# Optimization experiments

Hardware: AMD Instinct MI355X
Metric: run time of the kernel (lower is better)

## Reference

```python
import jax, jax.numpy as jnp
import numpy as np

FP8_E4M3_MAX = 448.0  # max representable magnitude of float8_e4m3fn

def fake_quant_fp8(t):
    """Per-tensor dynamic-scale fp8 (e4m3) quantize + dequantize."""
    amax = jnp.max(jnp.abs(t))
    scale = FP8_E4M3_MAX / jnp.maximum(amax, 1e-12)
    q = (t * scale).astype(jnp.float8_e4m3fn).astype(jnp.float32)
    return q / scale

def setup_inputs() -> dict:
    key = jax.random.key(0)
    k1, k2, k3 = jax.random.split(key, 3)
    d_in, d_out = 1024, 1024
    x = jax.random.normal(k1, (4, 8192, d_in), dtype=jnp.float32)
    weight = jax.random.normal(k2, (d_out, d_in), dtype=jnp.float32) * (1.0 / np.sqrt(d_in))
    bias = jax.random.normal(k3, (d_out,), dtype=jnp.float32) * 0.01
    return {"x": x, "weight": weight, "bias": bias}

def reference(x, weight, bias):
    # fp8-quantized linear: quantize activations and weights to e4m3 with
    # per-tensor dynamic scales, matmul, dequant (folded into fake-quant), add bias.
    xq = fake_quant_fp8(x)        # [b, s, d_in]
    wq = fake_quant_fp8(weight)   # [d_out, d_in]
    return jnp.einsum('bsd,od->bso', xq, wq) + bias
```

## Files before the change

kernel.cpp:

```cpp
#include <hip/hip_runtime.h>
#include <stdint.h>

typedef float floatx4 __attribute__((ext_vector_type(4)));
typedef int intx8 __attribute__((ext_vector_type(8)));

#define FP8_MAX 448.0f
#define BM 128
#define BN 128
#define BK 128
#define GX 2048
#define GW 256

__global__ void amax_partial(const float* __restrict__ x, long n4x,
                             const float* __restrict__ w, long n4w,
                             float* __restrict__ part) {
    const float4* p4; long n4, i0, stride;
    if (blockIdx.x < GX) {
        p4 = (const float4*)x; n4 = n4x;
        i0 = (long)blockIdx.x * blockDim.x + threadIdx.x;
        stride = (long)GX * blockDim.x;
    } else {
        p4 = (const float4*)w; n4 = n4w;
        i0 = (long)(blockIdx.x - GX) * blockDim.x + threadIdx.x;
        stride = (long)GW * blockDim.x;
    }
    float m = 0.f;
    for (long i = i0; i < n4; i += stride) {
        float4 v = p4[i];
        m = fmaxf(m, fmaxf(fmaxf(fabsf(v.x), fabsf(v.y)),
                           fmaxf(fabsf(v.z), fabsf(v.w))));
    }
    #pragma unroll
    for (int off = 32; off > 0; off >>= 1) m = fmaxf(m, __shfl_down(m, off, 64));
    __shared__ float red[4];
    if ((threadIdx.x & 63) == 0) red[threadIdx.x >> 6] = m;
    __syncthreads();
    if (threadIdx.x == 0)
        part[blockIdx.x] = fmaxf(fmaxf(red[0], red[1]), fmaxf(red[2], red[3]));
}

__global__ void quantw_scales(const float* __restrict__ part,
                              const float* __restrict__ w, int4* __restrict__ wq,
                              long n16w, float* __restrict__ scales) {
    const int tid = threadIdx.x;
    float mx = 0.f, mw = 0.f;
    for (int i = tid; i < GX; i += 256) mx = fmaxf(mx, part[i]);
    for (int i = GX + tid; i < GX + GW; i += 256) mw = fmaxf(mw, part[i]);
    #pragma unroll
    for (int off = 32; off > 0; off >>= 1) {
        mx = fmaxf(mx, __shfl_down(mx, off, 64));
        mw = fmaxf(mw, __shfl_down(mw, off, 64));
    }
    __shared__ float rx[4], rw[4];
    if ((tid & 63) == 0) { rx[tid >> 6] = mx; rw[tid >> 6] = mw; }
    __syncthreads();
    const float ax = fmaxf(fmaxf(rx[0], rx[1]), fmaxf(rx[2], rx[3]));
    const float aw = fmaxf(fmaxf(rw[0], rw[1]), fmaxf(rw[2], rw[3]));
    const float sx = FP8_MAX / fmaxf(ax, 1e-12f);
    const float sw = FP8_MAX / fmaxf(aw, 1e-12f);
    if (blockIdx.x == 0 && tid == 0) {
        scales[0] = sx; scales[1] = sw; scales[2] = 1.0f / (sx * sw);
    }
    const float4* p4 = (const float4*)w;
    const long i = (long)blockIdx.x * 256 + tid;
    if (i < n16w) {
        float4 v0 = p4[i * 4 + 0];
        float4 v1 = p4[i * 4 + 1];
        float4 v2 = p4[i * 4 + 2];
        float4 v3 = p4[i * 4 + 3];
        int w0 = 0, w1 = 0, w2 = 0, w3 = 0;
        w0 = __builtin_amdgcn_cvt_pk_fp8_f32(v0.x * sw, v0.y * sw, w0, false);
        w0 = __builtin_amdgcn_cvt_pk_fp8_f32(v0.z * sw, v0.w * sw, w0, true);
        w1 = __builtin_amdgcn_cvt_pk_fp8_f32(v1.x * sw, v1.y * sw, w1, false);
        w1 = __builtin_amdgcn_cvt_pk_fp8_f32(v1.z * sw, v1.w * sw, w1, true);
        w2 = __builtin_amdgcn_cvt_pk_fp8_f32(v2.x * sw, v2.y * sw, w2, false);
        w2 = __builtin_amdgcn_cvt_pk_fp8_f32(v2.z * sw, v2.w * sw, w2, true);
        w3 = __builtin_amdgcn_cvt_pk_fp8_f32(v3.x * sw, v3.y * sw, w3, false);
        w3 = __builtin_amdgcn_cvt_pk_fp8_f32(v3.z * sw, v3.w * sw, w3, true);
        wq[i] = make_int4(w0, w1, w2, w3);
    }
}

__global__ __launch_bounds__(256) void gemm_fp8mx(
    const float* __restrict__ xf, const unsigned char* __restrict__ Bq,
    const float* __restrict__ bias, const float* __restrict__ scales,
    float* __restrict__ out, int M, int N, int K) {
    __shared__ __align__(16) unsigned char tA[BM * BK];
    __shared__ __align__(16) unsigned char tB[BN * BK];

    const int tid = threadIdx.x;
    const int lane = tid & 63;
    const int wave = tid >> 6;
    const int waveM = (wave & 1) * 64;
    const int waveN = (wave >> 1) * 64;

    const int nbx = gridDim.x;
    const int nwg = nbx * gridDim.y;
    int bx = blockIdx.x, by = blockIdx.y;
    if (nbx == 8 && (nwg & 7) == 0) {
        const int f   = by * 8 + bx;
        const int per = nwg >> 3;
        const int sw  = (f & 7) * per + (f >> 3);
        bx = sw & 7;
        by = sw >> 3;
    }
    const long m0 = (long)by * BM;
    const int n0 = bx * BN;

    const int srow = lane >> 3;
    const int sphys = lane & 7;

    const float sx = scales[0];
    const float inv = scales[2];

    floatx4 acc[4][4];
    #pragma unroll
    for (int i = 0; i < 4; ++i)
        #pragma unroll
        for (int j = 0; j < 4; ++j)
            acc[i][j] = (floatx4){0.f, 0.f, 0.f, 0.f};

    const int row16 = lane & 15;
    const int q2 = (lane >> 4) * 2;

    const float4* x4 = (const float4*)xf;
    const int K4 = K >> 2;

    for (int k0 = 0; k0 < K; k0 += BK) {
        __syncthreads();
        #pragma unroll
        for (int c = 0; c < 4; ++c) {
            const int r = wave * 32 + c * 8 + srow;
            const int lc = (sphys ^ (r & 7)) * 16;
            __builtin_amdgcn_global_load_lds(
                (const __attribute__((address_space(1))) void*)(Bq + (long)(n0 + r) * K + k0 + lc),
                (__attribute__((address_space(3))) void*)&tB[r * BK + sphys * 16], 16, 0, 0);
        }
        #pragma unroll
        for (int j = 0; j < 4; ++j) {
            const int fidx = (tid << 2) + (j << 10);
            const int row = fidx >> 5;
            const int c4 = fidx & 31;
            const float4* px = x4 + (m0 + row) * (long)K4 + (k0 >> 2) + c4;
            const float4 v0 = px[0];
            const float4 v1 = px[1];
            const float4 v2 = px[2];
            const float4 v3 = px[3];
            int w0 = 0, w1 = 0, w2 = 0, w3 = 0;
            w0 = __builtin_amdgcn_cvt_pk_fp8_f32(v0.x * sx, v0.y * sx, w0, false);
            w0 = __builtin_amdgcn_cvt_pk_fp8_f32(v0.z * sx, v0.w * sx, w0, true);
            w1 = __builtin_amdgcn_cvt_pk_fp8_f32(v1.x * sx, v1.y * sx, w1, false);
            w1 = __builtin_amdgcn_cvt_pk_fp8_f32(v1.z * sx, v1.w * sx, w1, true);
            w2 = __builtin_amdgcn_cvt_pk_fp8_f32(v2.x * sx, v2.y * sx, w2, false);
            w2 = __builtin_amdgcn_cvt_pk_fp8_f32(v2.z * sx, v2.w * sx, w2, true);
            w3 = __builtin_amdgcn_cvt_pk_fp8_f32(v3.x * sx, v3.y * sx, w3, false);
            w3 = __builtin_amdgcn_cvt_pk_fp8_f32(v3.z * sx, v3.w * sx, w3, true);
            const int phys = (tid & 7) ^ (row & 7);
            *(int4*)&tA[row * BK + phys * 16] = make_int4(w0, w1, w2, w3);
        }
        __syncthreads();

        intx8 af[4], bf[4];
        #pragma unroll
        for (int t = 0; t < 4; ++t) {
            const int row = waveM + t * 16 + row16;
            const int s = row & 7;
            const int4 lo = *(const int4*)&tA[row * BK + ((q2 ^ s)) * 16];
            const int4 hi = *(const int4*)&tA[row * BK + (((q2 + 1) ^ s)) * 16];
            af[t] = (intx8){lo.x, lo.y, lo.z, lo.w, hi.x, hi.y, hi.z, hi.w};
        }
        #pragma unroll
        for (int t = 0; t < 4; ++t) {
            const int row = waveN + t * 16 + row16;
            const int s = row & 7;
            const int4 lo = *(const int4*)&tB[row * BK + ((q2 ^ s)) * 16];
            const int4 hi = *(const int4*)&tB[row * BK + (((q2 + 1) ^ s)) * 16];
            bf[t] = (intx8){lo.x, lo.y, lo.z, lo.w, hi.x, hi.y, hi.z, hi.w};
        }
        #pragma unroll
        for (int mt = 0; mt < 4; ++mt)
            #pragma unroll
            for (int nt = 0; nt < 4; ++nt)
                acc[mt][nt] = __builtin_amdgcn_mfma_scale_f32_16x16x128_f8f6f4(
                    af[mt], bf[nt], acc[mt][nt], 0, 0,
                    0, 127, 0, 127);
    }

    const int col = lane & 15;
    const int rbase4 = (lane >> 4) * 4;
    #pragma unroll
    for (int nt = 0; nt < 4; ++nt) {
        const int gn = n0 + waveN + nt * 16 + col;
        const float bv = bias[gn];
        #pragma unroll
        for (int mt = 0; mt < 4; ++mt) {
            const long gm = m0 + waveM + mt * 16 + rbase4;
            float* po = out + gm * (long)N + gn;
            #pragma unroll
            for (int r = 0; r < 4; ++r)
                po[(long)r * N] = acc[mt][nt][r] * inv + bv;
        }
    }
}

extern "C" void kernel_launch(void* const* d_in, const int* in_sizes, int n_in,
                              void* d_out, int out_size, void* d_ws, size_t ws_size,
                              hipStream_t stream) {
    const float* x = (const float*)d_in[0];
    const float* w = (const float*)d_in[1];
    const float* bias = (const float*)d_in[2];
    float* out = (float*)d_out;

    const long nx = in_sizes[0];
    const long nw = in_sizes[1];
    const int N = in_sizes[2];
    const long K = nw / N;
    const long M = nx / K;

    unsigned char* ws = (unsigned char*)d_ws;
    unsigned char* wq = ws;
    float* part = (float*)(ws + nw);
    float* scales = (float*)(ws + nw + 16384);

    amax_partial<<<GX + GW, 256, 0, stream>>>(x, nx / 4, w, nw / 4, part);
    quantw_scales<<<GW, 256, 0, stream>>>(part, w, (int4*)wq, nw / 16, scales);

    dim3 grid(N / BN, (int)(M / BM));
    gemm_fp8mx<<<grid, 256, 0, stream>>>(x, wq, bias, scales, out,
                                         (int)M, N, (int)K);
}
```

Baseline: 314.9 us.

## Software-pipeline fp32 activation loads into registers one K-tile ahead

Prefetches the next K-tile of fp32 activations into 16 float4 registers while the current tile is converted to fp8, stored to LDS and consumed by MFMAs. The syncthreads calls are replaced by explicit s_barrier with a partial vmcnt wait, so the outstanding global prefetch loads stay in flight across the barrier. This hides global load latency behind compute at the cost of 64 extra VGPRs per thread, which may lower occupancy. The hand-written waitcnt must match the exact number of outstanding loads, which adds fragility.

Result: no change. 309.8 us (-1.6%).

```diff
diff --git a/kernel.cpp b/kernel.cpp
--- a/kernel.cpp
+++ b/kernel.cpp
@@ -126,8 +126,22 @@
     const float4* x4 = (const float4*)xf;
     const int K4 = K >> 2;
 
+    const int arow0 = tid >> 3;
+    const int ac4   = (tid & 7) * 4;
+    const int aphys = tid & 7;
+
+    float4 pre[16];
+    #pragma unroll
+    for (int j = 0; j < 4; ++j) {
+        const int row = arow0 + 32 * j;
+        const float4* px = x4 + (m0 + row) * (long)K4 + ac4;
+        pre[j * 4 + 0] = px[0];
+        pre[j * 4 + 1] = px[1];
+        pre[j * 4 + 2] = px[2];
+        pre[j * 4 + 3] = px[3];
+    }
+
     for (int k0 = 0; k0 < K; k0 += BK) {
-        __syncthreads();
         #pragma unroll
         for (int c = 0; c < 4; ++c) {
             const int r = wave * 32 + c * 8 + srow;
@@ -136,16 +150,14 @@
                 (const __attribute__((address_space(1))) void*)(Bq + (long)(n0 + r) * K + k0 + lc),
                 (__attribute__((address_space(3))) void*)&tB[r * BK + sphys * 16], 16, 0, 0);
         }
+        __builtin_amdgcn_sched_barrier(0);
+
         #pragma unroll
         for (int j = 0; j < 4; ++j) {
-            const int fidx = (tid << 2) + (j << 10);
-            const int row = fidx >> 5;
-            const int c4 = fidx & 31;
-            const float4* px = x4 + (m0 + row) * (long)K4 + (k0 >> 2) + c4;
-            const float4 v0 = px[0];
-            const float4 v1 = px[1];
-            const float4 v2 = px[2];
-            const float4 v3 = px[3];
+            const float4 v0 = pre[j * 4 + 0];
+            const float4 v1 = pre[j * 4 + 1];
+            const float4 v2 = pre[j * 4 + 2];
+            const float4 v3 = pre[j * 4 + 3];
             int w0 = 0, w1 = 0, w2 = 0, w3 = 0;
             w0 = __builtin_amdgcn_cvt_pk_fp8_f32(v0.x * sx, v0.y * sx, w0, false);
             w0 = __builtin_amdgcn_cvt_pk_fp8_f32(v0.z * sx, v0.w * sx, w0, true);
@@ -155,10 +167,26 @@
             w2 = __builtin_amdgcn_cvt_pk_fp8_f32(v2.z * sx, v2.w * sx, w2, true);
             w3 = __builtin_amdgcn_cvt_pk_fp8_f32(v3.x * sx, v3.y * sx, w3, false);
             w3 = __builtin_amdgcn_cvt_pk_fp8_f32(v3.z * sx, v3.w * sx, w3, true);
-            const int phys = (tid & 7) ^ (row & 7);
+            const int row = arow0 + 32 * j;
+            const int phys = aphys ^ (row & 7);
             *(int4*)&tA[row * BK + phys * 16] = make_int4(w0, w1, w2, w3);
         }
-        __syncthreads();
+        __builtin_amdgcn_sched_barrier(0);
+
+        const int kn4 = ((k0 + BK < K) ? (k0 + BK) : k0) >> 2;
+        #pragma unroll
+        for (int j = 0; j < 4; ++j) {
+            const int row = arow0 + 32 * j;
+            const float4* px = x4 + (m0 + row) * (long)K4 + kn4 + ac4;
+            pre[j * 4 + 0] = px[0];
+            pre[j * 4 + 1] = px[1];
+            pre[j * 4 + 2] = px[2];
+            pre[j * 4 + 3] = px[3];
+        }
+
+        asm volatile("s_waitcnt vmcnt(16) lgkmcnt(0)" ::: "memory");
+        __builtin_amdgcn_s_barrier();
+        __builtin_amdgcn_sched_barrier(0);
 
         intx8 af[4], bf[4];
         #pragma unroll
@@ -184,6 +212,9 @@
                 acc[mt][nt] = __builtin_amdgcn_mfma_scale_f32_16x16x128_f8f6f4(
                     af[mt], bf[nt], acc[mt][nt], 0, 0,
                     0, 127, 0, 127);
+
+        __builtin_amdgcn_s_barrier();
+        __builtin_amdgcn_sched_barrier(0);
     }
 
     const int col = lane & 15;
```

## Software-pipeline the fp8 GEMM main loop with double-buffered B and register-prefetched A

Applied to the files above, without the earlier changes.

Restructures the K loop into a two-stage software pipeline. The B tile is double-buffered in LDS via async global_load_lds, and the fp32 activation tiles are prefetched two iterations ahead into two register arrays (preA and preB). Explicit vmcnt waits, s_barrier and sched_barrier calls order the stages so that global loads overlap with conversion and MFMA work. This adds about 128 VGPRs of prefetch storage and an extra 16KB of LDS, which may lower occupancy, and it relies on a hand-counted vmcnt value. It also assumes the number of K tiles is even.

Result: slower. 351.4 us (+11.6%).

```diff
diff --git a/kernel.cpp b/kernel.cpp
--- a/kernel.cpp
+++ b/kernel.cpp
@@ -86,7 +86,8 @@
     const float* __restrict__ bias, const float* __restrict__ scales,
     float* __restrict__ out, int M, int N, int K) {
     __shared__ __align__(16) unsigned char tA[BM * BK];
-    __shared__ __align__(16) unsigned char tB[BN * BK];
+    __shared__ __align__(16) unsigned char tB0[BN * BK];
+    __shared__ __align__(16) unsigned char tB1[BN * BK];
 
     const int tid = threadIdx.x;
     const int lane = tid & 63;
@@ -125,66 +126,117 @@
 
     const float4* x4 = (const float4*)xf;
     const int K4 = K >> 2;
-
-    for (int k0 = 0; k0 < K; k0 += BK) {
-        __syncthreads();
-        #pragma unroll
-        for (int c = 0; c < 4; ++c) {
-            const int r = wave * 32 + c * 8 + srow;
-            const int lc = (sphys ^ (r & 7)) * 16;
-            __builtin_amdgcn_global_load_lds(
-                (const __attribute__((address_space(1))) void*)(Bq + (long)(n0 + r) * K + k0 + lc),
-                (__attribute__((address_space(3))) void*)&tB[r * BK + sphys * 16], 16, 0, 0);
-        }
-        #pragma unroll
-        for (int j = 0; j < 4; ++j) {
-            const int fidx = (tid << 2) + (j << 10);
-            const int row = fidx >> 5;
-            const int c4 = fidx & 31;
-            const float4* px = x4 + (m0 + row) * (long)K4 + (k0 >> 2) + c4;
-            const float4 v0 = px[0];
-            const float4 v1 = px[1];
-            const float4 v2 = px[2];
-            const float4 v3 = px[3];
-            int w0 = 0, w1 = 0, w2 = 0, w3 = 0;
-            w0 = __builtin_amdgcn_cvt_pk_fp8_f32(v0.x * sx, v0.y * sx, w0, false);
-            w0 = __builtin_amdgcn_cvt_pk_fp8_f32(v0.z * sx, v0.w * sx, w0, true);
-            w1 = __builtin_amdgcn_cvt_pk_fp8_f32(v1.x * sx, v1.y * sx, w1, false);
-            w1 = __builtin_amdgcn_cvt_pk_fp8_f32(v1.z * sx, v1.w * sx, w1, true);
-            w2 = __builtin_amdgcn_cvt_pk_fp8_f32(v2.x * sx, v2.y * sx, w2, false);
-            w2 = __builtin_amdgcn_cvt_pk_fp8_f32(v2.z * sx, v2.w * sx, w2, true);
-            w3 = __builtin_amdgcn_cvt_pk_fp8_f32(v3.x * sx, v3.y * sx, w3, false);
-            w3 = __builtin_amdgcn_cvt_pk_fp8_f32(v3.z * sx, v3.w * sx, w3, true);
-            const int phys = (tid & 7) ^ (row & 7);
-            *(int4*)&tA[row * BK + phys * 16] = make_int4(w0, w1, w2, w3);
-        }
-        __syncthreads();
-
-        intx8 af[4], bf[4];
-        #pragma unroll
-        for (int t = 0; t < 4; ++t) {
-            const int row = waveM + t * 16 + row16;
-            const int s = row & 7;
-            const int4 lo = *(const int4*)&tA[row * BK + ((q2 ^ s)) * 16];
-            const int4 hi = *(const int4*)&tA[row * BK + (((q2 + 1) ^ s)) * 16];
-            af[t] = (intx8){lo.x, lo.y, lo.z, lo.w, hi.x, hi.y, hi.z, hi.w};
-        }
-        #pragma unroll
-        for (int t = 0; t < 4; ++t) {
-            const int row = waveN + t * 16 + row16;
-            const int s = row & 7;
-            const int4 lo = *(const int4*)&tB[row * BK + ((q2 ^ s)) * 16];
-            const int4 hi = *(const int4*)&tB[row * BK + (((q2 + 1) ^ s)) * 16];
-            bf[t] = (intx8){lo.x, lo.y, lo.z, lo.w, hi.x, hi.y, hi.z, hi.w};
-        }
-        #pragma unroll
-        for (int mt = 0; mt < 4; ++mt)
-            #pragma unroll
-            for (int nt = 0; nt < 4; ++nt)
-                acc[mt][nt] = __builtin_amdgcn_mfma_scale_f32_16x16x128_f8f6f4(
-                    af[mt], bf[nt], acc[mt][nt], 0, 0,
-                    0, 127, 0, 127);
-    }
+    const int KLAST = K - BK;
+
+    const int arow0 = tid >> 3;
+    const int ac4   = (tid & 7) * 4;
+    const int aphys = tid & 7;
+
+#define ISSUE_B(kt, tBdst) do {                                                     \
+    const int kb_ = (kt);                                                           \
+    _Pragma("unroll")                                                               \
+    for (int c = 0; c < 4; ++c) {                                                   \
+        const int r_ = wave * 32 + c * 8 + srow;                                    \
+        const int lc_ = (sphys ^ (r_ & 7)) * 16;                                    \
+        __builtin_amdgcn_global_load_lds(                                           \
+            (const __attribute__((address_space(1))) void*)(Bq + (long)(n0 + r_) * K + kb_ + lc_), \
+            (__attribute__((address_space(3))) void*)&(tBdst)[r_ * BK + sphys * 16], 16, 0, 0);    \
+    } } while (0)
+
+#define ISSUE_A(kt, pre) do {                                                       \
+    const int kq_ = (kt) >> 2;                                                      \
+    _Pragma("unroll")                                                               \
+    for (int j = 0; j < 4; ++j) {                                                   \
+        const int row_ = arow0 + 32 * j;                                            \
+        const float4* px_ = x4 + (m0 + row_) * (long)K4 + kq_ + ac4;                \
+        pre[j * 4 + 0] = px_[0];                                                    \
+        pre[j * 4 + 1] = px_[1];                                                    \
+        pre[j * 4 + 2] = px_[2];                                                    \
+        pre[j * 4 + 3] = px_[3];                                                    \
+    } } while (0)
+
+#define CVT_STORE(pre) do {                                                         \
+    _Pragma("unroll")                                                               \
+    for (int j = 0; j < 4; ++j) {                                                   \
+        const float4 v0_ = pre[j * 4 + 0];                                          \
+        const float4 v1_ = pre[j * 4 + 1];                                          \
+        const float4 v2_ = pre[j * 4 + 2];                                          \
+        const float4 v3_ = pre[j * 4 + 3];                                          \
+        int w0_ = 0, w1_ = 0, w2_ = 0, w3_ = 0;                                     \
+        w0_ = __builtin_amdgcn_cvt_pk_fp8_f32(v0_.x * sx, v0_.y * sx, w0_, false);  \
+        w0_ = __builtin_amdgcn_cvt_pk_fp8_f32(v0_.z * sx, v0_.w * sx, w0_, true);   \
+        w1_ = __builtin_amdgcn_cvt_pk_fp8_f32(v1_.x * sx, v1_.y * sx, w1_, false);  \
+        w1_ = __builtin_amdgcn_cvt_pk_fp8_f32(v1_.z * sx, v1_.w * sx, w1_, true);   \
+        w2_ = __builtin_amdgcn_cvt_pk_fp8_f32(v2_.x * sx, v2_.y * sx, w2_, false);  \
+        w2_ = __builtin_amdgcn_cvt_pk_fp8_f32(v2_.z * sx, v2_.w * sx, w2_, true);   \
+        w3_ = __builtin_amdgcn_cvt_pk_fp8_f32(v3_.x * sx, v3_.y * sx, w3_, false);  \
+        w3_ = __builtin_amdgcn_cvt_pk_fp8_f32(v3_.z * sx, v3_.w * sx, w3_, true);   \
+        const int row_ = arow0 + 32 * j;                                            \
+        const int phys_ = aphys ^ (row_ & 7);                                       \
+        *(int4*)&tA[row_ * BK + phys_ * 16] = make_int4(w0_, w1_, w2_, w3_);        \
+    } } while (0)
+
+#define FRAG_MFMA(tBcur) do {                                                       \
+    intx8 af_[4], bf_[4];                                                           \
+    _Pragma("unroll")                                                               \
+    for (int t_ = 0; t_ < 4; ++t_) {                                                \
+        const int row_ = waveM + t_ * 16 + row16;                                   \
+        const int s_ = row_ & 7;                                                    \
+        const int4 lo_ = *(const int4*)&tA[row_ * BK + ((q2 ^ s_)) * 16];           \
+        const int4 hi_ = *(const int4*)&tA[row_ * BK + (((q2 + 1) ^ s_)) * 16];     \
+        af_[t_] = (intx8){lo_.x, lo_.y, lo_.z, lo_.w, hi_.x, hi_.y, hi_.z, hi_.w};  \
+    }                                                                               \
+    _Pragma("unroll")                                                               \
+    for (int t_ = 0; t_ < 4; ++t_) {                                                \
+        const int row_ = waveN + t_ * 16 + row16;                                   \
+        const int s_ = row_ & 7;                                                    \
+        const int4 lo_ = *(const int4*)&(tBcur)[row_ * BK + ((q2 ^ s_)) * 16];      \
+        const int4 hi_ = *(const int4*)&(tBcur)[row_ * BK + (((q2 + 1) ^ s_)) * 16];\
+        bf_[t_] = (intx8){lo_.x, lo_.y, lo_.z, lo_.w, hi_.x, hi_.y, hi_.z, hi_.w};  \
+    }                                                                               \
+    _Pragma("unroll")                                                               \
+    for (int mt_ = 0; mt_ < 4; ++mt_)                                               \
+        _Pragma("unroll")                                                           \
+        for (int nt_ = 0; nt_ < 4; ++nt_)                                           \
+            acc[mt_][nt_] = __builtin_amdgcn_mfma_scale_f32_16x16x128_f8f6f4(       \
+                af_[mt_], bf_[nt_], acc[mt_][nt_], 0, 0, 0, 127, 0, 127);           \
+    } while (0)
+
+#define BODY(t, preCur, tBnext, tBcur) do {                                         \
+    const int ktB_ = ((t) + 1) * BK <= KLAST ? ((t) + 1) * BK : KLAST;              \
+    const int ktA_ = ((t) + 2) * BK <= KLAST ? ((t) + 2) * BK : KLAST;              \
+    ISSUE_B(ktB_, tBnext);                                                          \
+    __builtin_amdgcn_sched_barrier(0);                                              \
+    CVT_STORE(preCur);                                                              \
+    __builtin_amdgcn_sched_barrier(0);                                              \
+    ISSUE_A(ktA_, preCur);                                                          \
+    asm volatile("s_waitcnt vmcnt(36) lgkmcnt(0)" ::: "memory");                    \
+    __builtin_amdgcn_s_barrier();                                                   \
+    __builtin_amdgcn_sched_barrier(0);                                              \
+    FRAG_MFMA(tBcur);                                                               \
+    __builtin_amdgcn_s_barrier();                                                   \
+    __builtin_amdgcn_sched_barrier(0);                                              \
+} while (0)
+
+    float4 preA[16], preB[16];
+    ISSUE_B(0, tB0);
+    ISSUE_A(0, preA);
+    {
+        const int k1 = BK <= KLAST ? BK : KLAST;
+        ISSUE_A(k1, preB);
+    }
+
+    const int NT = K / BK;
+    for (int t = 0; t < NT; t += 2) {
+        BODY(t,     preA, tB1, tB0);
+        BODY(t + 1, preB, tB0, tB1);
+    }
+
+#undef BODY
+#undef FRAG_MFMA
+#undef CVT_STORE
+#undef ISSUE_A
+#undef ISSUE_B
 
     const int col = lane & 15;
     const int rbase4 = (lane >> 4) * 4;
```
